# Optimization experiments

Hardware: AMD Instinct MI355X
Metric: run time of the kernel (lower is better)

The kernel has to match this reference:

```python
import jax, jax.numpy as jnp
import numpy as np

N_NODES = 100000
N_EDGES = 1600000
IN_CH = 256
OUT_CH = 64
BN_EPS = 1e-5


def gcn_conv(x, edge_index, W, b, n_nodes):
    # PyG GCNConv: h = x @ W; add self-loops; symmetric normalization; scatter-add at dst; + bias
    h = x @ W  # [N, out]
    loop = jnp.arange(n_nodes, dtype=edge_index.dtype)
    src = jnp.concatenate([edge_index[0], loop])
    dst = jnp.concatenate([edge_index[1], loop])
    deg = jnp.zeros((n_nodes,), h.dtype).at[dst].add(jnp.ones((), h.dtype))
    dinv = jnp.where(deg > 0, jax.lax.rsqrt(deg), 0.0)
    norm = dinv[src] * dinv[dst]  # [E+N]
    msg = h[src] * norm[:, None]  # gather + scale
    out = jax.ops.segment_sum(msg, dst, num_segments=n_nodes)
    return out + b


def batch_norm(x, gamma, beta):
    mu = x.mean(axis=0)
    var = x.var(axis=0)  # biased, as torch BN training stats
    return (x - mu) * jax.lax.rsqrt(var + BN_EPS) * gamma + beta


def setup_inputs() -> dict:
    key = jax.random.key(0)
    ks = jax.random.split(key, 8)
    x = jax.random.normal(ks[0], (N_NODES, IN_CH), dtype=jnp.float32)
    edge_index = jax.random.randint(ks[1], (2, N_EDGES), 0, N_NODES, dtype=jnp.int32)
    def glorot(k, fan_in, fan_out):
        s = (6.0 / (fan_in + fan_out)) ** 0.5
        return jax.random.uniform(k, (fan_in, fan_out), jnp.float32, -s, s)
    return {
        "x": x,
        "edge_index": edge_index,
        "W1": glorot(ks[2], IN_CH, 128), "b1": jnp.zeros((128,), jnp.float32),
        "gamma1": jnp.ones((128,), jnp.float32), "beta1": jnp.zeros((128,), jnp.float32),
        "W2": glorot(ks[3], 128, 64), "b2": jnp.zeros((64,), jnp.float32),
        "gamma2": jnp.ones((64,), jnp.float32), "beta2": jnp.zeros((64,), jnp.float32),
        "W3": glorot(ks[4], 64, OUT_CH), "b3": jnp.zeros((OUT_CH,), jnp.float32),
    }


def reference(x, edge_index, W1, b1, gamma1, beta1, W2, b2, gamma2, beta2, W3, b3):
    n = x.shape[0]
    h = gcn_conv(x, edge_index, W1, b1, n)
    h = jax.nn.relu(batch_norm(h, gamma1, beta1))  # dropout = identity (eval)
    h = gcn_conv(h, edge_index, W2, b2, n)
    h = jax.nn.relu(batch_norm(h, gamma2, beta2))
    z = gcn_conv(h, edge_index, W3, b3, n)
    return z
```

## Files before the change

### kernel.cpp

```cpp
#include <hip/hip_runtime.h>
#include <cstdint>
#include <cstddef>

#define IN_CH 256

constexpr float BN_EPS = 1e-5f;

using u16x4 = __attribute__((ext_vector_type(4))) unsigned short;
using u16x8 = __attribute__((ext_vector_type(8))) unsigned short;
using bf16x8 = __attribute__((ext_vector_type(8))) short;
using f32x4 = __attribute__((ext_vector_type(4))) float;

__device__ __forceinline__ unsigned short f2bf_rne(float x) {
  unsigned u = __builtin_bit_cast(unsigned, x);
  unsigned r = u + 0x7FFFu + ((u >> 16) & 1u);
  return (unsigned short)(r >> 16);
}
__device__ __forceinline__ float bf2f(unsigned short h) {
  unsigned u = ((unsigned)h) << 16;
  return __builtin_bit_cast(float, u);
}
__device__ __forceinline__ float lo16f(unsigned u) {
  return __builtin_bit_cast(float, u << 16);
}
__device__ __forceinline__ float hi16f(unsigned u) {
  return __builtin_bit_cast(float, u & 0xffff0000u);
}


#define NBK_MAX 400

__global__ __launch_bounds__(256) void bucket_hist(const int* __restrict__ dst,
                                                   int* __restrict__ bcnt, int E, int nbk) {
  __shared__ int c[NBK_MAX];
  for (int j = threadIdx.x; j < nbk; j += 256) c[j] = 0;
  __syncthreads();
  for (int i = blockIdx.x * 256 + threadIdx.x; i < E; i += gridDim.x * 256)
    atomicAdd(&c[dst[i] >> 8], 1);
  __syncthreads();
  for (int j = threadIdx.x; j < nbk; j += 256)
    if (c[j]) atomicAdd(&bcnt[j], c[j]);
}

__global__ void bucket_scan(const int* __restrict__ bcnt, int* __restrict__ boff,
                            int* __restrict__ gcur, int E, int nbk) {
  __shared__ int lds[512];
  int t = threadIdx.x;
  int v = (t < nbk) ? bcnt[t] : 0;
  lds[t] = v;
  __syncthreads();
  for (int s = 1; s < 512; s <<= 1) {
    int x = (t >= s) ? lds[t - s] : 0;
    __syncthreads();
    lds[t] += x;
    __syncthreads();
  }
  if (t < nbk) {
    boff[t] = lds[t] - v;
    gcur[t] = lds[t] - v;
  }
  if (t == 0) boff[nbk] = E;
}

__global__ __launch_bounds__(256) void partition(const int* __restrict__ src,
                                                 const int* __restrict__ dst,
                                                 int* __restrict__ gcur,
                                                 unsigned* __restrict__ part, int E, int nbk) {
  __shared__ int cnt[NBK_MAX];
  __shared__ int base[NBK_MAX];
  const int t = threadIdx.x;
  for (int j = t; j < nbk; j += 256) cnt[j] = 0;
  __syncthreads();
  const int e0 = blockIdx.x * 4096;
  unsigned mypk[16];
  int mybk[16];
#pragma unroll
  for (int u = 0; u < 16; ++u) {
    int e = e0 + u * 256 + t;
    if (e < E) {
      int d = dst[e];
      mypk[u] = (unsigned)src[e] | ((unsigned)(d & 255) << 17);
      mybk[u] = d >> 8;
      atomicAdd(&cnt[mybk[u]], 1);
    } else {
      mybk[u] = -1;
    }
  }
  __syncthreads();
  for (int j = t; j < nbk; j += 256) {
    int c = cnt[j];
    base[j] = c ? atomicAdd(&gcur[j], c) : 0;
    cnt[j] = 0;
  }
  __syncthreads();
#pragma unroll
  for (int u = 0; u < 16; ++u) {
    if (mybk[u] >= 0) {
      int r = atomicAdd(&cnt[mybk[u]], 1);
      part[base[mybk[u]] + r] = mypk[u];
    }
  }
}

__global__ __launch_bounds__(256) void bucket_csr(const unsigned* __restrict__ part,
                                                  const int* __restrict__ boff,
                                                  int* __restrict__ offs, int* __restrict__ srcs,
                                                  float* __restrict__ dinv, int N, int E) {
  __shared__ unsigned pk[8192];
  __shared__ int ssrc[8192];
  __shared__ int cnt[256];
  __shared__ int offl[256];
  __shared__ int cur[256];
  const int b = blockIdx.x;
  const int t = threadIdx.x;
  const int e0 = boff[b];
  int ne = boff[b + 1] - e0;
  if (ne > 8192) ne = 8192;
  cnt[t] = 0;
  __syncthreads();
  for (int i = t; i < ne; i += 256) {
    unsigned v = part[e0 + i];
    pk[i] = v;
    atomicAdd(&cnt[v >> 17], 1);
  }
  __syncthreads();
  int vv = cnt[t];
  offl[t] = vv;
  __syncthreads();
  for (int s = 1; s < 256; s <<= 1) {
    int x = (t >= s) ? offl[t - s] : 0;
    __syncthreads();
    offl[t] += x;
    __syncthreads();
  }
  int excl = offl[t] - vv;
  cur[t] = excl;
  __syncthreads();
  for (int i = t; i < ne; i += 256) {
    unsigned p = pk[i];
    int dl = p >> 17;
    int r = atomicAdd(&cur[dl], 1);
    ssrc[r] = (int)(p & 0x1FFFF) << 5;
  }
  __syncthreads();
  for (int i = t; i < ne; i += 256) srcs[e0 + i] = ssrc[i];
  int node = b * 256 + t;
  if (node < N) {
    offs[node] = e0 + excl;
    dinv[node] = rsqrtf((float)(vv + 1));
  }
  if (b == gridDim.x - 1 && t == 0) offs[N] = E;
}


__global__ void wprep(const float* __restrict__ W, unsigned short* __restrict__ hi,
                      unsigned short* __restrict__ lo, int K, int N) {
  int i = blockIdx.x * 256 + threadIdx.x;
  if (i >= K * N) return;
  int k = i / N, n = i - k * N;
  float v = W[i];
  unsigned short h = f2bf_rne(v);
  hi[(size_t)n * K + k] = h;
  lo[(size_t)n * K + k] = f2bf_rne(v - bf2f(h));
}


template <int K, int BN, int SLICES, bool BNRELU, bool ABF16>
__global__ __launch_bounds__(256) void mfma_gemm(const void* __restrict__ Av,
                                                 const unsigned short* __restrict__ Bt_hi,
                                                 const unsigned short* __restrict__ Bt_lo,
                                                 const float* __restrict__ ss,
                                                 const float* __restrict__ dinv,
                                                 unsigned short* __restrict__ Out, int M) {
  constexpr int BM = 128;
  constexpr int CS = BN / SLICES;
  __shared__ unsigned short Ah[BM * 32];
  __shared__ unsigned short Al[BM * 32];
  __shared__ unsigned short Bh[BN * 32];
  __shared__ unsigned short Bl[BN * 32];

  const int tid = threadIdx.x;
  const int wave = tid >> 6;
  const int lane = tid & 63;
  const int lg = lane >> 4;
  const int lr = lane & 15;
  const int row0 = blockIdx.x * BM;

  f32x4 acc[2][BN / 16];
#pragma unroll
  for (int f = 0; f < 2; ++f)
#pragma unroll
    for (int j = 0; j < BN / 16; ++j) acc[f][j] = (f32x4){0.f, 0.f, 0.f, 0.f};

  for (int k0 = 0; k0 < K; k0 += 32) {
    __syncthreads();
#pragma unroll
    for (int it = 0; it < 4; ++it) {
      int m = it * 32 + (tid >> 3);
      int c2 = tid & 7;
      float vv[4] = {0.f, 0.f, 0.f, 0.f};
      if constexpr (ABF16) {
        if (row0 + m < M) {
          u16x4 r = *(const u16x4*)&(
              (const unsigned short*)Av)[(size_t)(row0 + m) * K + k0 + c2 * 4];
#pragma unroll
          for (int i = 0; i < 4; ++i) vv[i] = bf2f(r[i]);
        }
      } else {
        if (row0 + m < M) {
          float4 v = *(const float4*)&((const float*)Av)[(size_t)(row0 + m) * K + k0 + c2 * 4];
          vv[0] = v.x;
          vv[1] = v.y;
          vv[2] = v.z;
          vv[3] = v.w;
        }
      }
      if constexpr (BNRELU) {
        int kk = k0 + c2 * 4;
        float4 sc = *(const float4*)&ss[kk];
        float4 sh = *(const float4*)&ss[K + kk];
        vv[0] = fmaxf(0.f, fmaf(vv[0], sc.x, sh.x));
        vv[1] = fmaxf(0.f, fmaf(vv[1], sc.y, sh.y));
        vv[2] = fmaxf(0.f, fmaf(vv[2], sc.z, sh.z));
        vv[3] = fmaxf(0.f, fmaf(vv[3], sc.w, sh.w));
      }
      u16x4 h4, l4;
#pragma unroll
      for (int i = 0; i < 4; ++i) {
        unsigned short h = f2bf_rne(vv[i]);
        h4[i] = h;
        l4[i] = f2bf_rne(vv[i] - bf2f(h));
      }
      int pr = (m >> 1) & 3;
      int base = m * 32 + (((c2 >> 1) ^ pr) * 8) + (c2 & 1) * 4;
      *(u16x4*)&Ah[base] = h4;
      *(u16x4*)&Al[base] = l4;
    }
#pragma unroll
    for (int it = 0; it < BN / 64; ++it) {
      int n = it * 64 + (tid >> 2);
      int c = tid & 3;
      int pr = (n >> 1) & 3;
      int base = n * 32 + ((c ^ pr) * 8);
      *(u16x8*)&Bh[base] = *(const u16x8*)&Bt_hi[(size_t)n * K + k0 + c * 8];
      *(u16x8*)&Bl[base] = *(const u16x8*)&Bt_lo[(size_t)n * K + k0 + c * 8];
    }
    __syncthreads();

    bf16x8 afh[2], afl[2];
#pragma unroll
    for (int f = 0; f < 2; ++f) {
      int m = wave * 32 + f * 16 + lr;
      int pr = (m >> 1) & 3;
      int base = m * 32 + ((lg ^ pr) * 8);
      afh[f] = *(const bf16x8*)&Ah[base];
      afl[f] = *(const bf16x8*)&Al[base];
    }
#pragma unroll
    for (int j = 0; j < BN / 16; ++j) {
      int n = j * 16 + lr;
      int pr = (n >> 1) & 3;
      int base = n * 32 + ((lg ^ pr) * 8);
      bf16x8 bh = *(const bf16x8*)&Bh[base];
      bf16x8 bl = *(const bf16x8*)&Bl[base];
#pragma unroll
      for (int f = 0; f < 2; ++f) {
        acc[f][j] = __builtin_amdgcn_mfma_f32_16x16x32_bf16(afh[f], bh, acc[f][j], 0, 0, 0);
        acc[f][j] = __builtin_amdgcn_mfma_f32_16x16x32_bf16(afl[f], bh, acc[f][j], 0, 0, 0);
        acc[f][j] = __builtin_amdgcn_mfma_f32_16x16x32_bf16(afh[f], bl, acc[f][j], 0, 0, 0);
      }
    }
  }

#pragma unroll
  for (int f = 0; f < 2; ++f) {
#pragma unroll
    for (int r4 = 0; r4 < 4; ++r4) {
      int r = row0 + wave * 32 + f * 16 + lg * 4 + r4;
      if (r >= M) continue;
      float dv = dinv[r];
#pragma unroll
      for (int j = 0; j < BN / 16; ++j) {
        int c = j * 16 + lr;
        int slice = c / CS;
        int wi = c % CS;
        Out[((size_t)slice * M + r) * CS + wi] = f2bf_rne(acc[f][j][r4] * dv);
      }
    }
  }
}


template <int C, int NSLICE, bool STATS, bool FINAL>
__global__ __launch_bounds__(256) void agg_slice(const unsigned short* __restrict__ g,
                                                 const int* __restrict__ offs,
                                                 const int* __restrict__ srcsb,
                                                 const float* __restrict__ dinv,
                                                 const float* __restrict__ bias,
                                                 void* __restrict__ outv,
                                                 float* __restrict__ stat, int N) {
  constexpr int CS = C / NSLICE;
  constexpr int LPE = 8;
  constexpr int NPW = 64 / LPE;
  constexpr int T = 4;
  const int s = blockIdx.x;
  const int w = threadIdx.x >> 6;
  const int lane = threadIdx.x & 63;
  const int gi = lane >> 3;
  const int ch2 = lane & 7;
  const char* lane_base = (const char*)(g + (size_t)s * N * CS) + ch2 * 4;
  const int cb = ch2 * 2;

  float sx = 0.f, sy = 0.f, qx = 0.f, qy = 0.f;

#pragma unroll
  for (int it = 0; it < T; ++it) {
    int node = blockIdx.y * 128 + it * (4 * NPW) + w * NPW + gi;
    if (node < N) {
      unsigned u = *(const unsigned*)(lane_base + (size_t)node * (CS * 2));
      float ax = lo16f(u);
      float ay = hi16f(u);

      const int e0 = offs[node], e1 = offs[node + 1];
      const int nb = (e1 - e0 + 7) >> 3;
      int sA[8], sB[8];
#pragma unroll
      for (int j = 0; j < 8; ++j) sA[j] = srcsb[e0 + j];
      for (int b = 0; b < nb; ++b) {
        const int base = e0 + b * 8;
#pragma unroll
        for (int j = 0; j < 8; ++j) sB[j] = srcsb[base + 8 + j];
        unsigned uu[8];
#pragma unroll
        for (int j = 0; j < 8; ++j) {
          uu[j] = 0u;
          if (base + j < e1) uu[j] = *(const unsigned*)(lane_base + (size_t)(unsigned)sA[j]);
        }
#pragma unroll
        for (int j = 0; j < 8; ++j) {
          ax += lo16f(uu[j]);
          ay += hi16f(uu[j]);
        }
#pragma unroll
        for (int j = 0; j < 8; ++j) sA[j] = sB[j];
      }
      float dv = dinv[node];
      float ox = ax * dv, oy = ay * dv;
      if constexpr (FINAL) {
        ox += bias[s * CS + cb];
        oy += bias[s * CS + cb + 1];
        *(float2*)&((float*)outv)[(size_t)node * C + s * CS + cb] = (float2){ox, oy};
      } else {
        unsigned ob = (unsigned)f2bf_rne(ox) | ((unsigned)f2bf_rne(oy) << 16);
        ((unsigned*)outv)[((size_t)node * C + s * CS + cb) >> 1] = ob;
      }
      if constexpr (STATS) {
        sx += ox;
        sy += oy;
        qx += ox * ox;
        qy += oy * oy;
      }
    }
  }

  if constexpr (STATS) {
    __shared__ float red[256][4];
    red[threadIdx.x][0] = sx;
    red[threadIdx.x][1] = sy;
    red[threadIdx.x][2] = qx;
    red[threadIdx.x][3] = qy;
    __syncthreads();
    if (threadIdx.x < LPE) {
      float a0 = 0.f, a1 = 0.f, a2 = 0.f, a3 = 0.f;
      for (int k = threadIdx.x; k < 256; k += LPE) {
        a0 += red[k][0];
        a1 += red[k][1];
        a2 += red[k][2];
        a3 += red[k][3];
      }
      atomicAdd(&stat[s * CS + threadIdx.x * 2], a0);
      atomicAdd(&stat[s * CS + threadIdx.x * 2 + 1], a1);
      atomicAdd(&stat[C + s * CS + threadIdx.x * 2], a2);
      atomicAdd(&stat[C + s * CS + threadIdx.x * 2 + 1], a3);
    }
  }
}


template <int C>
__global__ void bn_finalize(const float* __restrict__ stat, const float* __restrict__ gamma,
                            const float* __restrict__ beta, float* __restrict__ ss, int N) {
  int c = threadIdx.x;
  if (c >= C) return;
  float mu = stat[c] / (float)N;
  float var = stat[C + c] / (float)N - mu * mu;
  float rs = rsqrtf(var + BN_EPS);
  float sc = gamma[c] * rs;
  ss[c] = sc;
  ss[C + c] = beta[c] - mu * sc;
}


extern "C" void kernel_launch(void* const* d_in, const int* in_sizes, int n_in, void* d_out,
                              int out_size, void* d_ws, size_t ws_size, hipStream_t stream) {
  const float* x = (const float*)d_in[0];
  const int* ei = (const int*)d_in[1];
  const float* W1 = (const float*)d_in[2];
  const float* gamma1 = (const float*)d_in[4];
  const float* beta1 = (const float*)d_in[5];
  const float* W2 = (const float*)d_in[6];
  const float* gamma2 = (const float*)d_in[8];
  const float* beta2 = (const float*)d_in[9];
  const float* W3 = (const float*)d_in[10];
  const float* b3 = (const float*)d_in[11];
  float* out = (float*)d_out;

  const int N = in_sizes[0] / IN_CH;
  const int E = in_sizes[1] / 2;
  const int* e_src = ei;
  const int* e_dst = ei + E;
  const int nbk = (N + 255) >> 8;

  char* ws = (char*)d_ws;
  size_t off = 0;
  auto alloc = [&](size_t bytes) {
    size_t r = off;
    off += (bytes + 1023) & ~(size_t)1023;
    return r;
  };
  int* bcnt = (int*)(ws + alloc(NBK_MAX * 4));
  int* boff = (int*)(ws + alloc((NBK_MAX + 1) * 4));
  int* gcur = (int*)(ws + alloc(NBK_MAX * 4));
  unsigned* part = (unsigned*)(ws + alloc((size_t)E * 4));
  int* offs = (int*)(ws + alloc((size_t)(N + 1) * 4));
  int* srcs = (int*)(ws + alloc(((size_t)E + 32) * 4));
  float* dinv = (float*)(ws + alloc((size_t)N * 4));
  unsigned short* Wt1h = (unsigned short*)(ws + alloc(256 * 128 * 2));
  unsigned short* Wt1l = (unsigned short*)(ws + alloc(256 * 128 * 2));
  unsigned short* Wt2h = (unsigned short*)(ws + alloc(128 * 64 * 2));
  unsigned short* Wt2l = (unsigned short*)(ws + alloc(128 * 64 * 2));
  unsigned short* Wt3h = (unsigned short*)(ws + alloc(64 * 64 * 2));
  unsigned short* Wt3l = (unsigned short*)(ws + alloc(64 * 64 * 2));
  float* stat1 = (float*)(ws + alloc(256 * 4));
  float* stat2 = (float*)(ws + alloc(128 * 4));
  float* ss1 = (float*)(ws + alloc(256 * 4));
  float* ss2 = (float*)(ws + alloc(128 * 4));
  unsigned short* g = (unsigned short*)(ws + alloc((size_t)N * 128 * 2));
  unsigned short* hb = (unsigned short*)(ws + alloc((size_t)N * 128 * 2));

  hipMemsetAsync(bcnt, 0, NBK_MAX * 4, stream);
  hipMemsetAsync(stat1, 0, 256 * 4, stream);
  hipMemsetAsync(stat2, 0, 128 * 4, stream);

  bucket_hist<<<2048, 256, 0, stream>>>(e_dst, bcnt, E, nbk);
  bucket_scan<<<1, 512, 0, stream>>>(bcnt, boff, gcur, E, nbk);
  partition<<<(E + 4095) / 4096, 256, 0, stream>>>(e_src, e_dst, gcur, part, E, nbk);
  bucket_csr<<<nbk, 256, 0, stream>>>(part, boff, offs, srcs, dinv, N, E);

  wprep<<<(256 * 128 + 255) / 256, 256, 0, stream>>>(W1, Wt1h, Wt1l, 256, 128);
  wprep<<<(128 * 64 + 255) / 256, 256, 0, stream>>>(W2, Wt2h, Wt2l, 128, 64);
  wprep<<<(64 * 64 + 255) / 256, 256, 0, stream>>>(W3, Wt3h, Wt3l, 64, 64);

  const int gM = (N + 127) / 128;
  const int nch = (N + 127) / 128;
  const dim3 gAgg1(8, nch);
  const dim3 gAgg2(4, nch);

  mfma_gemm<256, 128, 8, false, false><<<gM, 256, 0, stream>>>(x, Wt1h, Wt1l, nullptr, dinv, g,
                                                               N);
  agg_slice<128, 8, true, false><<<gAgg1, 256, 0, stream>>>(g, offs, srcs, dinv, nullptr, hb,
                                                            stat1, N);
  bn_finalize<128><<<1, 128, 0, stream>>>(stat1, gamma1, beta1, ss1, N);

  mfma_gemm<128, 64, 4, true, true><<<gM, 256, 0, stream>>>(hb, Wt2h, Wt2l, ss1, dinv, g, N);
  agg_slice<64, 4, true, false><<<gAgg2, 256, 0, stream>>>(g, offs, srcs, dinv, nullptr, hb,
                                                           stat2, N);
  bn_finalize<64><<<1, 64, 0, stream>>>(stat2, gamma2, beta2, ss2, N);

  mfma_gemm<64, 64, 4, true, true><<<gM, 256, 0, stream>>>(hb, Wt3h, Wt3l, ss2, dinv, g, N);
  agg_slice<64, 4, false, true><<<gAgg2, 256, 0, stream>>>(g, offs, srcs, dinv, b3, out, nullptr,
                                                           N);
}
```

Measured before the change: 376.9 us.

## Pad CSR neighbor lists to batches of eight with sentinel zero row

```diff
diff --git a/kernel.cpp b/kernel.cpp
--- a/kernel.cpp
+++ b/kernel.cpp
@@ -11,6 +11,16 @@
 using bf16x8 = __attribute__((ext_vector_type(8))) short;
 using f32x4 = __attribute__((ext_vector_type(4))) float;
 
+#if defined(__has_builtin)
+#if __has_builtin(__builtin_amdgcn_make_buffer_rsrc) && \
+    __has_builtin(__builtin_amdgcn_raw_buffer_load_b32)
+#define USE_BUFLOAD 1
+#endif
+#endif
+#ifndef USE_BUFLOAD
+#define USE_BUFLOAD 0
+#endif
+
 __device__ __forceinline__ unsigned short f2bf_rne(float x) {
   unsigned u = __builtin_bit_cast(unsigned, x);
   unsigned r = u + 0x7FFFu + ((u >> 16) & 1u);
@@ -29,6 +39,7 @@
 
 
 #define NBK_MAX 400
+#define BKT_RSV 2048
 
 __global__ __launch_bounds__(256) void bucket_hist(const int* __restrict__ dst,
                                                    int* __restrict__ bcnt, int E, int nbk) {
@@ -104,10 +115,12 @@
 
 __global__ __launch_bounds__(256) void bucket_csr(const unsigned* __restrict__ part,
                                                   const int* __restrict__ boff,
-                                                  int* __restrict__ offs, int* __restrict__ srcs,
+                                                  int* __restrict__ offs,
+                                                  unsigned char* __restrict__ nbat,
+                                                  int* __restrict__ srcs,
                                                   float* __restrict__ dinv, int N, int E) {
   __shared__ unsigned pk[8192];
-  __shared__ int ssrc[8192];
+  __shared__ int ssrc[8192 + BKT_RSV];
   __shared__ int cnt[256];
   __shared__ int offl[256];
   __shared__ int cur[256];
@@ -116,6 +129,7 @@
   const int e0 = boff[b];
   int ne = boff[b + 1] - e0;
   if (ne > 8192) ne = 8192;
+  const int e0p = e0 + b * BKT_RSV;
   cnt[t] = 0;
   __syncthreads();
   for (int i = t; i < ne; i += 256) {
@@ -124,8 +138,9 @@
     atomicAdd(&cnt[v >> 17], 1);
   }
   __syncthreads();
-  int vv = cnt[t];
-  offl[t] = vv;
+  const int deg = cnt[t];
+  const int degp = (deg + 7) & ~7;
+  offl[t] = degp;
   __syncthreads();
   for (int s = 1; s < 256; s <<= 1) {
     int x = (t >= s) ? offl[t - s] : 0;
@@ -133,23 +148,31 @@
     offl[t] += x;
     __syncthreads();
   }
-  int excl = offl[t] - vv;
-  cur[t] = excl;
+  const int exclp = offl[t] - degp;
+  const int totalp = offl[255];
+  cur[t] = exclp;
+  __syncthreads();
+  for (int i = t; i < totalp; i += 256) ssrc[i] = N << 5;
   __syncthreads();
   for (int i = t; i < ne; i += 256) {
     unsigned p = pk[i];
     int dl = p >> 17;
     int r = atomicAdd(&cur[dl], 1);
-    ssrc[r] = (int)(p & 0x1FFFF) << 5;
-  }
-  __syncthreads();
-  for (int i = t; i < ne; i += 256) srcs[e0 + i] = ssrc[i];
+    ssrc[r] = (int)((p & 0x1FFFFu) << 5);
+  }
+  __syncthreads();
+  for (int i = t; i < totalp; i += 256) srcs[e0p + i] = ssrc[i];
   int node = b * 256 + t;
   if (node < N) {
-    offs[node] = e0 + excl;
-    dinv[node] = rsqrtf((float)(vv + 1));
-  }
-  if (b == gridDim.x - 1 && t == 0) offs[N] = E;
+    offs[node] = e0p + exclp;
+    nbat[node] = (unsigned char)(degp >> 3);
+    dinv[node] = rsqrtf((float)(deg + 1));
+  }
+}
+
+__global__ void zrow(unsigned short* g, int N) {
+  int i = threadIdx.x;
+  if (i < 8 * 16) g[((size_t)(i >> 4) * (N + 1) + N) * 16 + (i & 15)] = 0;
 }
 
 
@@ -284,7 +307,7 @@
         int c = j * 16 + lr;
         int slice = c / CS;
         int wi = c % CS;
-        Out[((size_t)slice * M + r) * CS + wi] = f2bf_rne(acc[f][j][r4] * dv);
+        Out[((size_t)slice * (M + 1) + r) * CS + wi] = f2bf_rne(acc[f][j][r4] * dv);
       }
     }
   }
@@ -294,6 +317,7 @@
 template <int C, int NSLICE, bool STATS, bool FINAL>
 __global__ __launch_bounds__(256) void agg_slice(const unsigned short* __restrict__ g,
                                                  const int* __restrict__ offs,
+                                                 const unsigned char* __restrict__ nbat,
                                                  const int* __restrict__ srcsb,
                                                  const float* __restrict__ dinv,
                                                  const float* __restrict__ bias,
@@ -301,49 +325,63 @@
                                                  float* __restrict__ stat, int N) {
   constexpr int CS = C / NSLICE;
   constexpr int LPE = 8;
-  constexpr int NPW = 64 / LPE;
-  constexpr int T = 4;
   const int s = blockIdx.x;
   const int w = threadIdx.x >> 6;
   const int lane = threadIdx.x & 63;
   const int gi = lane >> 3;
   const int ch2 = lane & 7;
-  const char* lane_base = (const char*)(g + (size_t)s * N * CS) + ch2 * 4;
+  const unsigned choff = (unsigned)ch2 * 4;
+  const unsigned sliceBytes = (unsigned)(N + 1) * 32;
+  const char* sbase = (const char*)g + (size_t)s * sliceBytes;
   const int cb = ch2 * 2;
 
+#if USE_BUFLOAD
+  auto rsrc =
+      __builtin_amdgcn_make_buffer_rsrc((void*)sbase, (short)0, (int)sliceBytes, 0x00020000);
+  auto GATHER = [&](unsigned off) -> unsigned {
+    return (unsigned)__builtin_amdgcn_raw_buffer_load_b32(rsrc, (int)off, 0, 0);
+  };
+#else
+  auto GATHER = [&](unsigned off) -> unsigned {
+    return (off + 4 <= sliceBytes) ? *(const unsigned*)(sbase + off) : 0u;
+  };
+#endif
+
   float sx = 0.f, sy = 0.f, qx = 0.f, qy = 0.f;
 
 #pragma unroll
-  for (int it = 0; it < T; ++it) {
-    int node = blockIdx.y * 128 + it * (4 * NPW) + w * NPW + gi;
+  for (int it = 0; it < 4; ++it) {
+    int node = blockIdx.y * 128 + it * 32 + w * 8 + gi;
     if (node < N) {
-      unsigned u = *(const unsigned*)(lane_base + (size_t)node * (CS * 2));
+      unsigned u = *(const unsigned*)(sbase + (size_t)node * 32 + choff);
       float ax = lo16f(u);
       float ay = hi16f(u);
 
-      const int e0 = offs[node], e1 = offs[node + 1];
-      const int nb = (e1 - e0 + 7) >> 3;
-      int sA[8], sB[8];
-#pragma unroll
-      for (int j = 0; j < 8; ++j) sA[j] = srcsb[e0 + j];
+      const int base = offs[node];
+      const int nb = nbat[node];
+      unsigned sA[8], sB[8], gA[8], gB[8];
+#pragma unroll
+      for (int j = 0; j < 8; ++j) sA[j] = (unsigned)srcsb[base + j] | choff;
+#pragma unroll
+      for (int j = 0; j < 8; ++j) gA[j] = GATHER(sA[j]);
+#pragma unroll
+      for (int j = 0; j < 8; ++j) sB[j] = (unsigned)srcsb[base + 8 + j] | choff;
+
       for (int b = 0; b < nb; ++b) {
-        const int base = e0 + b * 8;
-#pragma unroll
-        for (int j = 0; j < 8; ++j) sB[j] = srcsb[base + 8 + j];
-        unsigned uu[8];
+#pragma unroll
+        for (int j = 0; j < 8; ++j) gB[j] = GATHER(sB[j]);
+#pragma unroll
+        for (int j = 0; j < 8; ++j)
+          sB[j] = (unsigned)srcsb[base + (b + 2) * 8 + j] | choff;
 #pragma unroll
         for (int j = 0; j < 8; ++j) {
-          uu[j] = 0u;
-          if (base + j < e1) uu[j] = *(const unsigned*)(lane_base + (size_t)(unsigned)sA[j]);
+          ax += lo16f(gA[j]);
+          ay += hi16f(gA[j]);
         }
 #pragma unroll
-        for (int j = 0; j < 8; ++j) {
-          ax += lo16f(uu[j]);
-          ay += hi16f(uu[j]);
-        }
-#pragma unroll
-        for (int j = 0; j < 8; ++j) sA[j] = sB[j];
-      }
+        for (int j = 0; j < 8; ++j) gA[j] = gB[j];
+      }
+
       float dv = dinv[node];
       float ox = ax * dv, oy = ay * dv;
       if constexpr (FINAL) {
@@ -433,7 +471,8 @@
   int* gcur = (int*)(ws + alloc(NBK_MAX * 4));
   unsigned* part = (unsigned*)(ws + alloc((size_t)E * 4));
   int* offs = (int*)(ws + alloc((size_t)(N + 1) * 4));
-  int* srcs = (int*)(ws + alloc(((size_t)E + 32) * 4));
+  int* srcs = (int*)(ws + alloc(((size_t)E + (size_t)nbk * BKT_RSV + 64) * 4));
+  unsigned char* nbat = (unsigned char*)(ws + alloc((size_t)N));
   float* dinv = (float*)(ws + alloc((size_t)N * 4));
   unsigned short* Wt1h = (unsigned short*)(ws + alloc(256 * 128 * 2));
   unsigned short* Wt1l = (unsigned short*)(ws + alloc(256 * 128 * 2));
@@ -445,7 +484,8 @@
   float* stat2 = (float*)(ws + alloc(128 * 4));
   float* ss1 = (float*)(ws + alloc(256 * 4));
   float* ss2 = (float*)(ws + alloc(128 * 4));
-  unsigned short* g = (unsigned short*)(ws + alloc((size_t)N * 128 * 2));
+  unsigned short* g =
+      (unsigned short*)(ws + alloc((size_t)8 * (N + 1) * 16 * 2));
   unsigned short* hb = (unsigned short*)(ws + alloc((size_t)N * 128 * 2));
 
   hipMemsetAsync(bcnt, 0, NBK_MAX * 4, stream);
@@ -455,7 +495,8 @@
   bucket_hist<<<2048, 256, 0, stream>>>(e_dst, bcnt, E, nbk);
   bucket_scan<<<1, 512, 0, stream>>>(bcnt, boff, gcur, E, nbk);
   partition<<<(E + 4095) / 4096, 256, 0, stream>>>(e_src, e_dst, gcur, part, E, nbk);
-  bucket_csr<<<nbk, 256, 0, stream>>>(part, boff, offs, srcs, dinv, N, E);
+  bucket_csr<<<nbk, 256, 0, stream>>>(part, boff, offs, nbat, srcs, dinv, N, E);
+  zrow<<<1, 128, 0, stream>>>(g, N);
 
   wprep<<<(256 * 128 + 255) / 256, 256, 0, stream>>>(W1, Wt1h, Wt1l, 256, 128);
   wprep<<<(128 * 64 + 255) / 256, 256, 0, stream>>>(W2, Wt2h, Wt2l, 128, 64);
@@ -468,16 +509,16 @@
 
   mfma_gemm<256, 128, 8, false, false><<<gM, 256, 0, stream>>>(x, Wt1h, Wt1l, nullptr, dinv, g,
                                                                N);
-  agg_slice<128, 8, true, false><<<gAgg1, 256, 0, stream>>>(g, offs, srcs, dinv, nullptr, hb,
-                                                            stat1, N);
+  agg_slice<128, 8, true, false><<<gAgg1, 256, 0, stream>>>(g, offs, nbat, srcs, dinv, nullptr,
+                                                            hb, stat1, N);
   bn_finalize<128><<<1, 128, 0, stream>>>(stat1, gamma1, beta1, ss1, N);
 
   mfma_gemm<128, 64, 4, true, true><<<gM, 256, 0, stream>>>(hb, Wt2h, Wt2l, ss1, dinv, g, N);
-  agg_slice<64, 4, true, false><<<gAgg2, 256, 0, stream>>>(g, offs, srcs, dinv, nullptr, hb,
-                                                           stat2, N);
+  agg_slice<64, 4, true, false><<<gAgg2, 256, 0, stream>>>(g, offs, nbat, srcs, dinv, nullptr,
+                                                           hb, stat2, N);
   bn_finalize<64><<<1, 64, 0, stream>>>(stat2, gamma2, beta2, ss2, N);
 
   mfma_gemm<64, 64, 4, true, true><<<gM, 256, 0, stream>>>(hb, Wt3h, Wt3l, ss2, dinv, g, N);
-  agg_slice<64, 4, false, true><<<gAgg2, 256, 0, stream>>>(g, offs, srcs, dinv, b3, out, nullptr,
-                                                           N);
-}
+  agg_slice<64, 4, false, true><<<gAgg2, 256, 0, stream>>>(g, offs, nbat, srcs, dinv, b3, out,
+                                                           nullptr, N);
+}
```

New measurement: 434.1 us. +15.2%, slower.
